# Kernel optimization log

Hardware: AMD Instinct MI355X
Metric: run time of the kernel (lower is better)

## Reference

```python
import jax, jax.numpy as jnp
import numpy as np

# Equal-time-constant (tau_mem == tau_syn) closed-form spike time, as in
# fastAndDeep utils_spiketime_et: for each causal set of the k earliest input
# spikes, t = tau * (b/a - W0(-c/a * exp(b/a))), with
#   a = sum_k w_k exp(t_k/tau),  b = sum_k w_k t_k exp(t_k/tau) / tau,
#   c = (threshold - leak) * g_leak.
TAU = 1.0
THRESHOLD = 1.0
LEAK = 0.0
G_LEAK = 1.0
INV_E = float(np.exp(-1.0))


def lambertw0(z):
    """Principal-branch Lambert W for z in [-1/e, 0), via Halley iterations."""
    z = jnp.clip(z, -INV_E + 1e-8, -1e-30)
    # branch-point expansion near -1/e, series z(1-z) elsewhere
    w = jnp.where(z < -0.2,
                  -1.0 + jnp.sqrt(2.0 * (1.0 + jnp.e * z)),
                  z * (1.0 - z))
    for _ in range(12):
        ew = jnp.exp(w)
        f = w * ew - z
        wp1 = w + 1.0
        w = w - f / (ew * wp1 - (w + 2.0) * f / (2.0 * wp1))
    return w


def setup_inputs() -> dict:
    key = jax.random.key(0)
    k1, k2 = jax.random.split(key)
    B, NPRE, NPOST = 128, 1024, 256
    # spike times in units of tau, all finite
    input_spikes = jax.random.uniform(k1, (B, NPRE), dtype=jnp.float32)
    # positive weights scaled so many neurons cross threshold
    input_weights = jax.random.uniform(k2, (NPRE, NPOST), dtype=jnp.float32) * 0.1
    return {"input_spikes": input_spikes, "input_weights": input_weights}


def reference(input_spikes, input_weights):
    # input_spikes: (B, NPRE), input_weights: (NPRE, NPOST)
    sort_idx = jnp.argsort(input_spikes, axis=1)                       # (B, NPRE)
    sorted_spikes = jnp.take_along_axis(input_spikes, sort_idx, axis=1)
    sorted_w = input_weights[sort_idx]                                 # (B, NPRE, NPOST)

    inf_mask = jnp.isinf(sorted_spikes)
    s = jnp.where(inf_mask, 0.0, sorted_spikes)[..., None]             # (B, NPRE, 1)
    sw = jnp.where(inf_mask[..., None], 0.0, sorted_w)

    e = jnp.exp(s / TAU)
    a = jnp.cumsum(sw * e, axis=1)                                     # (B, NPRE, NPOST)
    b = jnp.cumsum(sw * s * e, axis=1) / TAU
    c = (THRESHOLD - LEAK) * G_LEAK

    a_safe = jnp.where(jnp.abs(a) > 1e-10, a, 1e-10)
    z = -c / a_safe * jnp.exp(jnp.clip(b / a_safe, -30.0, 30.0))
    valid = (a > 0) & (z >= -INV_E)
    t = TAU * (b / a_safe - lambertw0(z))
    t = jnp.where(valid, t, jnp.inf)                                   # candidate spike times

    # causal-set consistency: spike must be after the k-th sorted input and
    # not later than the (k+1)-th sorted input (last row exempt)
    ss = sorted_spikes[..., None]
    not_after_last = t < ss
    next_spike = jnp.roll(sorted_spikes, -1, axis=1)[..., None]
    not_earlier_than_next = (t > next_spike).at[:, -1, :].set(False)
    t = jnp.where(not_after_last | not_earlier_than_next, jnp.inf, t)

    output_spikes = jnp.min(t, axis=1)                                 # (B, NPOST)
    return output_spikes
```

## Files before the change

### kernel.cpp

```cpp
#include <hip/hip_runtime.h>
#include <math.h>

#define BATCH 128
#define NPRE  1024
#define NPOST 256
#define NJB   128
#define NW    16
#define KPW   16
#define CLEN  256
#define NCHK  4

__device__ __forceinline__ float lambertw0_f(float z) {
    const float INV_E = 0.36787944117144233f;
    float zc = fminf(fmaxf(z, -INV_E + 1e-8f), -1e-30f);
    float w;
    if (zc < -0.2f) {
        w = -1.0f + sqrtf(2.0f * (1.0f + 2.718281828459045f * zc));
    } else {
        w = zc * (1.0f - zc);
    }
#pragma unroll
    for (int it = 0; it < 5; ++it) {
        float ew  = expf(w);
        float f   = w * ew - zc;
        float wp1 = w + 1.0f;
        w = w - f / (ew * wp1 - (w + 2.0f) * f / (2.0f * wp1));
    }
    return w;
}

__global__ __launch_bounds__(1024, 4)
void ttfs_kernel(const float* __restrict__ spikes,
                 const float* __restrict__ Wt,
                 float* __restrict__ out)
{
    __shared__ int    cnt[1024];
    __shared__ int    bstart[1025];
    __shared__ int    wsum[NW];
    __shared__ unsigned long long tmp64[NPRE];
    __shared__ float2 tse[NPRE + 1];
    __shared__ float2 tez[NPRE + 1];
    __shared__ int    sidx[NPRE + 4];
    __shared__ float  pA[NW][NJB + 2], pB[NW][NJB + 2];
    __shared__ int    flags[2];

    const int tid  = threadIdx.x;
    const int lane = tid & 63;
    const int wid  = tid >> 6;
    const int b    = (int)blockIdx.x >> 1;
    const int h    = (int)blockIdx.x & 1;

    {
        float s = spikes[b * NPRE + tid];
        unsigned long long v =
            (((unsigned long long)__float_as_uint(s)) << 32) | (unsigned)tid;
        int bucket = (int)(s * 1024.0f);
        bucket = bucket < 0 ? 0 : (bucket > 1023 ? 1023 : bucket);

        cnt[tid] = 0;
        __syncthreads();
        int arr = atomicAdd(&cnt[bucket], 1);
        __syncthreads();

        int c0 = cnt[tid];
        int x  = c0;
#pragma unroll
        for (int d = 1; d < 64; d <<= 1) {
            int y = __shfl_up(x, d);
            if (lane >= d) x += y;
        }
        if (lane == 63) wsum[wid] = x;
        __syncthreads();
        int ws = (lane < NW) ? wsum[lane] : 0;
#pragma unroll
        for (int d = 1; d < NW; d <<= 1) {
            int y = __shfl_up(ws, d);
            if (lane >= d) ws += y;
        }
        int base = (wid == 0) ? 0 : __shfl(ws, wid - 1);
        bstart[tid] = base + x - c0;
        if (tid == 0) bstart[1024] = NPRE;
        __syncthreads();

        int slot = bstart[bucket] + arr;
        tmp64[slot] = v;
        __syncthreads();

        int st = bstart[bucket], en = bstart[bucket + 1];
        int rk = 0;
        for (int q = st; q < en; ++q) rk += (tmp64[q] < v);
        int fin = st + rk;

        float e = expf(s);
        tse[fin]  = make_float2(s, e);
        tez[fin]  = make_float2(e, s * e);
        sidx[fin] = tid;
    }
    if (tid == 0) {
        tse[NPRE]  = make_float2(INFINITY, INFINITY);
        tez[NPRE]  = make_float2(INFINITY, 0.0f);
        sidx[NPRE] = 0; sidx[NPRE + 1] = 0; sidx[NPRE + 2] = 0; sidx[NPRE + 3] = 0;
    }
    __syncthreads();

    const int j0 = h * NJB;
    const float* __restrict__ Wc0 = Wt + j0 + lane;
    const float* __restrict__ Wc1 = Wt + j0 + 64 + lane;
    const int4* __restrict__ sidx4 = (const int4*)sidx;
    const int kbase = wid * KPW;

    float offA = 0.0f, offB = 0.0f;
    float preA = 0.0f, preB = 0.0f;
    int   baseK = -1;
    bool  doneJ = false;

#define LOADW2(kstart, dst)                                                   \
    {                                                                         \
        int4 Ia = sidx4[((kstart) >> 2) + 0];                                 \
        int4 Ib = sidx4[((kstart) >> 2) + 1];                                 \
        int4 Ic = sidx4[((kstart) >> 2) + 2];                                 \
        int4 Id = sidx4[((kstart) >> 2) + 3];                                 \
        dst[0]  = Wc0[Ia.x * NPOST]; dst[1]  = Wc0[Ia.y * NPOST];             \
        dst[2]  = Wc0[Ia.z * NPOST]; dst[3]  = Wc0[Ia.w * NPOST];             \
        dst[4]  = Wc0[Ib.x * NPOST]; dst[5]  = Wc0[Ib.y * NPOST];             \
        dst[6]  = Wc0[Ib.z * NPOST]; dst[7]  = Wc0[Ib.w * NPOST];             \
        dst[8]  = Wc0[Ic.x * NPOST]; dst[9]  = Wc0[Ic.y * NPOST];             \
        dst[10] = Wc0[Ic.z * NPOST]; dst[11] = Wc0[Ic.w * NPOST];             \
        dst[12] = Wc0[Id.x * NPOST]; dst[13] = Wc0[Id.y * NPOST];             \
        dst[14] = Wc0[Id.z * NPOST]; dst[15] = Wc0[Id.w * NPOST];             \
        dst[16] = Wc1[Ia.x * NPOST]; dst[17] = Wc1[Ia.y * NPOST];             \
        dst[18] = Wc1[Ia.z * NPOST]; dst[19] = Wc1[Ia.w * NPOST];             \
        dst[20] = Wc1[Ib.x * NPOST]; dst[21] = Wc1[Ib.y * NPOST];             \
        dst[22] = Wc1[Ib.z * NPOST]; dst[23] = Wc1[Ib.w * NPOST];             \
        dst[24] = Wc1[Ic.x * NPOST]; dst[25] = Wc1[Ic.y * NPOST];             \
        dst[26] = Wc1[Ic.z * NPOST]; dst[27] = Wc1[Ic.w * NPOST];             \
        dst[28] = Wc1[Id.x * NPOST]; dst[29] = Wc1[Id.y * NPOST];             \
        dst[30] = Wc1[Id.z * NPOST]; dst[31] = Wc1[Id.w * NPOST];             \
    }

    float wv[2 * KPW];
    LOADW2(kbase, wv);

    for (int ch = 0; ch < NCHK; ++ch) {
        const int kk0 = ch * CLEN + kbase;
        float a0 = 0.0f, b0 = 0.0f, a1 = 0.0f, b1 = 0.0f;
#pragma unroll
        for (int i = 0; i < KPW; ++i) {
            float2 t = tez[kk0 + i];
            a0 = fmaf(wv[i],       t.x, a0);
            b0 = fmaf(wv[i],       t.y, b0);
            a1 = fmaf(wv[KPW + i], t.x, a1);
            b1 = fmaf(wv[KPW + i], t.y, b1);
        }
        pA[wid][lane]      = a0; pB[wid][lane]      = b0;
        pA[wid][64 + lane] = a1; pB[wid][64 + lane] = b1;
        __syncthreads();

        if (wid < 2) {
            const int n = (wid << 6) + lane;
#pragma unroll
            for (int w = 0; w < NW; ++w) {
                float nA = offA + pA[w][n];
                float nB = offB + pB[w][n];
                if (!doneJ) {
                    float2 tn = tse[ch * CLEN + (w + 1) * KPW];
                    float gate = fmaf(nA, tn.x, -nB);
                    if (gate >= tn.y) {
                        baseK = ch * CLEN + w * KPW;
                        preA = offA; preB = offB;
                        doneJ = true;
                    }
                }
                offA = nA; offB = nB;
            }
            bool all = __all(doneJ);
            if (lane == 0) flags[wid] = all ? 1 : 0;
        }
        __syncthreads();
        if (flags[0] & flags[1]) break;
        if (ch < NCHK - 1) LOADW2(kk0 + CLEN, wv);
    }

    if (wid < 2) {
        const int n = (wid << 6) + lane;
        const float* __restrict__ Wcol = Wt + j0 + n;
        float result = INFINITY;
        const float INV_E = 0.36787944117144233f;
        if (doneJ) {
            float wl[KPW];
#pragma unroll
            for (int i = 0; i < KPW; ++i) wl[i] = Wcol[sidx[baseK + i] * NPOST];
            float A = preA, Bq = preB;
            int fk = -1; float fA = 0.0f, fB = 0.0f;
#pragma unroll
            for (int i = 0; i < KPW; ++i) {
                const int k = baseK + i;
                float2 ez = tez[k];
                A  = fmaf(wl[i], ez.x, A);
                Bq = fmaf(wl[i], ez.y, Bq);
                if (fk < 0) {
                    float2 tn = tse[k + 1];
                    float gate = fmaf(A, tn.x, -Bq);
                    if (gate >= tn.y) { fA = A; fB = Bq; fk = k; }
                }
            }

            if (fk >= 0) {
                float r   = fB / fA;
                float ezz = expf(fminf(fmaxf(r, -30.0f), 30.0f));
                float z   = -ezz / fA;
                bool valid = (fA > 0.0f) && (z >= -INV_E);
                float t = r - lambertw0_f(z);
                bool ok = valid && (t >= tse[fk].x) &&
                          (fk == NPRE - 1 || t <= tse[fk + 1].x);
                if (ok) {
                    result = t;
                } else {
                    float A2 = fA, B2 = fB;
                    for (int k = fk + 1; k < NPRE; ++k) {
                        float w = Wcol[sidx[k] * NPOST];
                        float2 ez2v = tez[k];
                        A2 = fmaf(w, ez2v.x, A2);
                        B2 = fmaf(w, ez2v.y, B2);
                        if (A2 <= 0.0f) continue;
                        float r2  = B2 / A2;
                        float ex2 = expf(fminf(fmaxf(r2, -30.0f), 30.0f));
                        float z2  = -ex2 / A2;
                        if (z2 < -INV_E) continue;
                        float t2 = r2 - lambertw0_f(z2);
                        if (t2 < tse[k].x) continue;
                        if (k < NPRE - 1 && t2 > tse[k + 1].x) continue;
                        result = t2;
                        break;
                    }
                }
            } else {
                float A2 = 0.0f, B2 = 0.0f;
                for (int k = 0; k < NPRE; ++k) {
                    float w = Wcol[sidx[k] * NPOST];
                    float2 ez2v = tez[k];
                    A2 = fmaf(w, ez2v.x, A2);
                    B2 = fmaf(w, ez2v.y, B2);
                    if (A2 <= 0.0f) continue;
                    float r2  = B2 / A2;
                    float ex2 = expf(fminf(fmaxf(r2, -30.0f), 30.0f));
                    float z2  = -ex2 / A2;
                    if (z2 < -INV_E) continue;
                    float t2 = r2 - lambertw0_f(z2);
                    if (t2 < tse[k].x) continue;
                    if (k < NPRE - 1 && t2 > tse[k + 1].x) continue;
                    result = t2;
                    break;
                }
            }
        }
        out[b * NPOST + j0 + n] = result;
    }
}

extern "C" void kernel_launch(void* const* d_in, const int* in_sizes, int n_in,
                              void* d_out, int out_size, void* d_ws, size_t ws_size,
                              hipStream_t stream) {
    const float* spikes  = (const float*)d_in[0];
    const float* weights = (const float*)d_in[1];
    float* outp = (float*)d_out;
    ttfs_kernel<<<dim3(BATCH * 2), dim3(1024), 0, stream>>>(spikes, weights, outp);
}
```

Measured before the change: 12.85 us.

## Vectorize weight gathers as float2 and parallelize final 16-step scan across block

```diff
diff --git a/kernel.cpp b/kernel.cpp
--- a/kernel.cpp
+++ b/kernel.cpp
@@ -43,6 +43,8 @@
     __shared__ int    sidx[NPRE + 4];
     __shared__ float  pA[NW][NJB + 2], pB[NW][NJB + 2];
     __shared__ int    flags[2];
+    __shared__ int    rbaseK[NJB];
+    __shared__ float  rpreA[NJB], rpreB[NJB];
 
     const int tid  = threadIdx.x;
     const int lane = tid & 63;
@@ -104,8 +106,6 @@
     __syncthreads();
 
     const int j0 = h * NJB;
-    const float* __restrict__ Wc0 = Wt + j0 + lane;
-    const float* __restrict__ Wc1 = Wt + j0 + 64 + lane;
     const int4* __restrict__ sidx4 = (const int4*)sidx;
     const int kbase = wid * KPW;
 
@@ -114,31 +114,24 @@
     int   baseK = -1;
     bool  doneJ = false;
 
+#define LW2(idx) (*(const float2*)(Wt + (idx) * NPOST + j0 + 2 * lane))
 #define LOADW2(kstart, dst)                                                   \
     {                                                                         \
         int4 Ia = sidx4[((kstart) >> 2) + 0];                                 \
         int4 Ib = sidx4[((kstart) >> 2) + 1];                                 \
         int4 Ic = sidx4[((kstart) >> 2) + 2];                                 \
         int4 Id = sidx4[((kstart) >> 2) + 3];                                 \
-        dst[0]  = Wc0[Ia.x * NPOST]; dst[1]  = Wc0[Ia.y * NPOST];             \
-        dst[2]  = Wc0[Ia.z * NPOST]; dst[3]  = Wc0[Ia.w * NPOST];             \
-        dst[4]  = Wc0[Ib.x * NPOST]; dst[5]  = Wc0[Ib.y * NPOST];             \
-        dst[6]  = Wc0[Ib.z * NPOST]; dst[7]  = Wc0[Ib.w * NPOST];             \
-        dst[8]  = Wc0[Ic.x * NPOST]; dst[9]  = Wc0[Ic.y * NPOST];             \
-        dst[10] = Wc0[Ic.z * NPOST]; dst[11] = Wc0[Ic.w * NPOST];             \
-        dst[12] = Wc0[Id.x * NPOST]; dst[13] = Wc0[Id.y * NPOST];             \
-        dst[14] = Wc0[Id.z * NPOST]; dst[15] = Wc0[Id.w * NPOST];             \
-        dst[16] = Wc1[Ia.x * NPOST]; dst[17] = Wc1[Ia.y * NPOST];             \
-        dst[18] = Wc1[Ia.z * NPOST]; dst[19] = Wc1[Ia.w * NPOST];             \
-        dst[20] = Wc1[Ib.x * NPOST]; dst[21] = Wc1[Ib.y * NPOST];             \
-        dst[22] = Wc1[Ib.z * NPOST]; dst[23] = Wc1[Ib.w * NPOST];             \
-        dst[24] = Wc1[Ic.x * NPOST]; dst[25] = Wc1[Ic.y * NPOST];             \
-        dst[26] = Wc1[Ic.z * NPOST]; dst[27] = Wc1[Ic.w * NPOST];             \
-        dst[28] = Wc1[Id.x * NPOST]; dst[29] = Wc1[Id.y * NPOST];             \
-        dst[30] = Wc1[Id.z * NPOST]; dst[31] = Wc1[Id.w * NPOST];             \
-    }
-
-    float wv[2 * KPW];
+        dst[0]  = LW2(Ia.x); dst[1]  = LW2(Ia.y);                             \
+        dst[2]  = LW2(Ia.z); dst[3]  = LW2(Ia.w);                             \
+        dst[4]  = LW2(Ib.x); dst[5]  = LW2(Ib.y);                             \
+        dst[6]  = LW2(Ib.z); dst[7]  = LW2(Ib.w);                             \
+        dst[8]  = LW2(Ic.x); dst[9]  = LW2(Ic.y);                             \
+        dst[10] = LW2(Ic.z); dst[11] = LW2(Ic.w);                             \
+        dst[12] = LW2(Id.x); dst[13] = LW2(Id.y);                             \
+        dst[14] = LW2(Id.z); dst[15] = LW2(Id.w);                             \
+    }
+
+    float2 wv[KPW];
     LOADW2(kbase, wv);
 
     for (int ch = 0; ch < NCHK; ++ch) {
@@ -147,17 +140,17 @@
 #pragma unroll
         for (int i = 0; i < KPW; ++i) {
             float2 t = tez[kk0 + i];
-            a0 = fmaf(wv[i],       t.x, a0);
-            b0 = fmaf(wv[i],       t.y, b0);
-            a1 = fmaf(wv[KPW + i], t.x, a1);
-            b1 = fmaf(wv[KPW + i], t.y, b1);
-        }
-        pA[wid][lane]      = a0; pB[wid][lane]      = b0;
-        pA[wid][64 + lane] = a1; pB[wid][64 + lane] = b1;
+            a0 = fmaf(wv[i].x, t.x, a0);
+            b0 = fmaf(wv[i].x, t.y, b0);
+            a1 = fmaf(wv[i].y, t.x, a1);
+            b1 = fmaf(wv[i].y, t.y, b1);
+        }
+        pA[wid][2 * lane]     = a0; pB[wid][2 * lane]     = b0;
+        pA[wid][2 * lane + 1] = a1; pB[wid][2 * lane + 1] = b1;
         __syncthreads();
 
         if (wid < 2) {
-            const int n = (wid << 6) + lane;
+            const int n = 2 * lane + wid;
 #pragma unroll
             for (int w = 0; w < NW; ++w) {
                 float nA = offA + pA[w][n];
@@ -182,46 +175,62 @@
     }
 
     if (wid < 2) {
-        const int n = (wid << 6) + lane;
-        const float* __restrict__ Wcol = Wt + j0 + n;
-        float result = INFINITY;
+        const int n = 2 * lane + wid;
+        rbaseK[n] = baseK; rpreA[n] = preA; rpreB[n] = preB;
+    }
+    __syncthreads();
+
+    {
+        const int q  = lane >> 3;
+        const int sl = lane & 7;
+        const int n  = (wid << 3) + q;
+        const float* __restrict__ Wn = Wt + j0 + n;
         const float INV_E = 0.36787944117144233f;
-        if (doneJ) {
-            float wl[KPW];
-#pragma unroll
-            for (int i = 0; i < KPW; ++i) wl[i] = Wcol[sidx[baseK + i] * NPOST];
-            float A = preA, Bq = preB;
-            int fk = -1; float fA = 0.0f, fB = 0.0f;
-#pragma unroll
-            for (int i = 0; i < KPW; ++i) {
-                const int k = baseK + i;
-                float2 ez = tez[k];
-                A  = fmaf(wl[i], ez.x, A);
-                Bq = fmaf(wl[i], ez.y, Bq);
-                if (fk < 0) {
-                    float2 tn = tse[k + 1];
-                    float gate = fmaf(A, tn.x, -Bq);
-                    if (gate >= tn.y) { fA = A; fB = Bq; fk = k; }
-                }
+        const int bK = rbaseK[n];
+
+        bool has = false;
+        int myfk = 0; float myA = 0.0f, myB = 0.0f;
+        if (bK >= 0) {
+            const int k0 = bK + 2 * sl;
+            float w0 = Wn[sidx[k0] * NPOST];
+            float w1 = Wn[sidx[k0 + 1] * NPOST];
+            float2 e0 = tez[k0], e1 = tez[k0 + 1];
+            float la = w0 * e0.x; la = fmaf(w1, e1.x, la);
+            float lb = w0 * e0.y; lb = fmaf(w1, e1.y, lb);
+            float sa = la, sb = lb;
+#pragma unroll
+            for (int d = 1; d < 8; d <<= 1) {
+                float ua = __shfl_up(sa, d, 8);
+                float ub = __shfl_up(sb, d, 8);
+                if (sl >= d) { sa += ua; sb += ub; }
             }
-
-            if (fk >= 0) {
-                float r   = fB / fA;
-                float ezz = expf(fminf(fmaxf(r, -30.0f), 30.0f));
-                float z   = -ezz / fA;
-                bool valid = (fA > 0.0f) && (z >= -INV_E);
-                float t = r - lambertw0_f(z);
-                bool ok = valid && (t >= tse[fk].x) &&
-                          (fk == NPRE - 1 || t <= tse[fk + 1].x);
-                if (ok) {
-                    result = t;
-                } else {
-                    float A2 = fA, B2 = fB;
-                    for (int k = fk + 1; k < NPRE; ++k) {
-                        float w = Wcol[sidx[k] * NPOST];
-                        float2 ez2v = tez[k];
-                        A2 = fmaf(w, ez2v.x, A2);
-                        B2 = fmaf(w, ez2v.y, B2);
+            float exA = rpreA[n] + (sa - la);
+            float exB = rpreB[n] + (sb - lb);
+            float A0 = fmaf(w0, e0.x, exA);
+            float B0 = fmaf(w0, e0.y, exB);
+            float A1 = fmaf(w1, e1.x, A0);
+            float B1 = fmaf(w1, e1.y, B0);
+            float2 t1 = tse[k0 + 1];
+            float2 t2 = tse[k0 + 2];
+            bool g0 = fmaf(A0, t1.x, -B0) >= t1.y;
+            bool g1 = fmaf(A1, t2.x, -B1) >= t2.y;
+            has  = g0 || g1;
+            myfk = g0 ? k0 : (k0 + 1);
+            myA  = g0 ? A0 : A1;
+            myB  = g0 ? B0 : B1;
+        }
+        unsigned long long bal = __ballot(has);
+        if (bK >= 0) {
+            unsigned mask8 = (unsigned)((bal >> (q * 8)) & 0xFFull);
+            if (mask8 == 0u) {
+                if (sl == 0) {
+                    float result = INFINITY;
+                    float A2 = 0.0f, B2 = 0.0f;
+                    for (int k = 0; k < NPRE; ++k) {
+                        float w = Wn[sidx[k] * NPOST];
+                        float2 ezv = tez[k];
+                        A2 = fmaf(w, ezv.x, A2);
+                        B2 = fmaf(w, ezv.y, B2);
                         if (A2 <= 0.0f) continue;
                         float r2  = B2 / A2;
                         float ex2 = expf(fminf(fmaxf(r2, -30.0f), 30.0f));
@@ -233,28 +242,46 @@
                         result = t2;
                         break;
                     }
+                    out[b * NPOST + j0 + n] = result;
                 }
             } else {
-                float A2 = 0.0f, B2 = 0.0f;
-                for (int k = 0; k < NPRE; ++k) {
-                    float w = Wcol[sidx[k] * NPOST];
-                    float2 ez2v = tez[k];
-                    A2 = fmaf(w, ez2v.x, A2);
-                    B2 = fmaf(w, ez2v.y, B2);
-                    if (A2 <= 0.0f) continue;
-                    float r2  = B2 / A2;
-                    float ex2 = expf(fminf(fmaxf(r2, -30.0f), 30.0f));
-                    float z2  = -ex2 / A2;
-                    if (z2 < -INV_E) continue;
-                    float t2 = r2 - lambertw0_f(z2);
-                    if (t2 < tse[k].x) continue;
-                    if (k < NPRE - 1 && t2 > tse[k + 1].x) continue;
-                    result = t2;
-                    break;
+                int f = __ffs((int)mask8) - 1;
+                if (sl == f) {
+                    float result = INFINITY;
+                    float r   = myB / myA;
+                    float ezz = expf(fminf(fmaxf(r, -30.0f), 30.0f));
+                    float z   = -ezz / myA;
+                    bool valid = (myA > 0.0f) && (z >= -INV_E);
+                    float t = r - lambertw0_f(z);
+                    bool ok = valid && (t >= tse[myfk].x) &&
+                              (myfk == NPRE - 1 || t <= tse[myfk + 1].x);
+                    if (ok) {
+                        result = t;
+                    } else {
+                        float A2 = myA, B2 = myB;
+                        for (int k = myfk + 1; k < NPRE; ++k) {
+                            float w = Wn[sidx[k] * NPOST];
+                            float2 ezv = tez[k];
+                            A2 = fmaf(w, ezv.x, A2);
+                            B2 = fmaf(w, ezv.y, B2);
+                            if (A2 <= 0.0f) continue;
+                            float r2  = B2 / A2;
+                            float ex2 = expf(fminf(fmaxf(r2, -30.0f), 30.0f));
+                            float z2  = -ex2 / A2;
+                            if (z2 < -INV_E) continue;
+                            float t2 = r2 - lambertw0_f(z2);
+                            if (t2 < tse[k].x) continue;
+                            if (k < NPRE - 1 && t2 > tse[k + 1].x) continue;
+                            result = t2;
+                            break;
+                        }
+                    }
+                    out[b * NPOST + j0 + n] = result;
                 }
             }
-        }
-        out[b * NPOST + j0 + n] = result;
+        } else if (sl == 0) {
+            out[b * NPOST + j0 + n] = INFINITY;
+        }
     }
 }
 
```

After: 14.52 us. +12.9%, slower.
